# Performance work log

Hardware: AMD Instinct MI355X
Metric: run time of the kernel (lower is better)

## Reference

```python
import jax, jax.numpy as jnp
import numpy as np

N_GRID, N_MESH, N_EDGE, H = 65536, 10242, 131072, 512

def _layernorm(x, g, b, eps=1e-5):
    m = jnp.mean(x, axis=-1, keepdims=True)
    v = jnp.var(x, axis=-1, keepdims=True)
    return (x - m) * jax.lax.rsqrt(v + eps) * g + b

def _mlp(x, W1, b1, W2, b2, g, b):
    # Linear -> SiLU -> Linear -> LayerNorm (GraphCast MeshGraphMLP)
    h = jax.nn.silu(x @ W1 + b1)
    return _layernorm(h @ W2 + b2, g, b)

def setup_inputs() -> dict:
    key = jax.random.key(0)
    ks = jax.random.split(key, 16)
    s = lambda fan_in: 1.0 / np.sqrt(fan_in)
    inp = {
        'grid_node_features': jax.random.normal(ks[0], (N_GRID, H), jnp.float32),
        'mesh_node_features': jax.random.normal(ks[1], (N_MESH, H), jnp.float32),
        'grid2mesh_edge_features': jax.random.normal(ks[2], (N_EDGE, H), jnp.float32),
        'src_indices': jax.random.randint(ks[3], (N_EDGE,), 0, N_GRID),
        'dst_indices': jax.random.randint(ks[4], (N_EDGE,), 0, N_MESH),
        # edge MLP: in = concat(edge, src, dst) = 3H
        'We1': jax.random.normal(ks[5], (3 * H, H), jnp.float32) * s(3 * H),
        'be1': jnp.zeros((H,), jnp.float32),
        'We2': jax.random.normal(ks[6], (H, H), jnp.float32) * s(H),
        'be2': jnp.zeros((H,), jnp.float32),
        'ge': jnp.ones((H,), jnp.float32), 'bbe': jnp.zeros((H,), jnp.float32),
        # node MLP: in = concat(node, agg) = 2H
        'Wn1': jax.random.normal(ks[7], (2 * H, H), jnp.float32) * s(2 * H),
        'bn1': jnp.zeros((H,), jnp.float32),
        'Wn2': jax.random.normal(ks[8], (H, H), jnp.float32) * s(H),
        'bn2': jnp.zeros((H,), jnp.float32),
        'gn': jnp.ones((H,), jnp.float32), 'bbn': jnp.zeros((H,), jnp.float32),
        # grid node MLP: H -> H
        'Wg1': jax.random.normal(ks[9], (H, H), jnp.float32) * s(H),
        'bg1': jnp.zeros((H,), jnp.float32),
        'Wg2': jax.random.normal(ks[10], (H, H), jnp.float32) * s(H),
        'bg2': jnp.zeros((H,), jnp.float32),
        'gg': jnp.ones((H,), jnp.float32), 'bbg': jnp.zeros((H,), jnp.float32),
    }
    return inp

def reference(grid_node_features, mesh_node_features, grid2mesh_edge_features,
              src_indices, dst_indices,
              We1, be1, We2, be2, ge, bbe,
              Wn1, bn1, Wn2, bn2, gn, bbn,
              Wg1, bg1, Wg2, bg2, gg, bbg):
    # --- MeshEdgeBlock: gather src/dst, concat, MLP, residual on edges ---
    cat_e = jnp.concatenate([grid2mesh_edge_features,
                             grid_node_features[src_indices],
                             mesh_node_features[dst_indices]], axis=-1)  # [E, 3H]
    e_feats = grid2mesh_edge_features + _mlp(cat_e, We1, be1, We2, be2, ge, bbe)
    # --- MeshNodeBlock: scatter-sum edges to mesh nodes, concat, MLP ---
    agg = jax.ops.segment_sum(e_feats, dst_indices, num_segments=N_MESH)  # [M, H]
    cat_n = jnp.concatenate([mesh_node_features, agg], axis=-1)  # [M, 2H]
    n_feats = _mlp(cat_n, Wn1, bn1, Wn2, bn2, gn, bbn)
    mesh_out = mesh_node_features + n_feats
    # --- grid node MLP + residual ---
    grid_out = grid_node_features + _mlp(grid_node_features, Wg1, bg1, Wg2, bg2, gg, bbg)
    return (grid_out, mesh_out)
```

## Files before the change

kernel.cpp:

```cpp
#include <hip/hip_runtime.h>
#include <stdint.h>

typedef unsigned short u16;
typedef unsigned int   u32;
typedef unsigned char  u8;

using bf16x8 = __attribute__((ext_vector_type(8))) short;
using f32x4  = __attribute__((ext_vector_type(4))) float;

#define DEVF static __device__ __forceinline__

DEVF u16 f2bf(float f){
  u32 u = __builtin_bit_cast(u32, f);
  u32 r = u + 0x7FFFu + ((u >> 16) & 1u);
  return (u16)(r >> 16);
}
DEVF float bf2f(u16 h){
  u32 u = ((u32)h) << 16;
  return __builtin_bit_cast(float, u);
}

DEVF void gload_lds16(const u16* g, u16* s){
  __builtin_amdgcn_global_load_lds(
      (const __attribute__((address_space(1))) u32*)g,
      (__attribute__((address_space(3))) u32*)(u32)(uintptr_t)s,
      16, 0, 0);
}


__global__ __launch_bounds__(256) void k_f32_to_bf16(const float* __restrict__ in,
                                                     u16* __restrict__ out, long n){
  long i = (long)blockIdx.x * blockDim.x + threadIdx.x;
  long stride = (long)gridDim.x * blockDim.x;
  for (long j = i * 8; j < n; j += stride * 8){
    float4 a = *(const float4*)(in + j);
    float4 b = *(const float4*)(in + j + 4);
    bf16x8 v;
    v[0]=(short)f2bf(a.x); v[1]=(short)f2bf(a.y); v[2]=(short)f2bf(a.z); v[3]=(short)f2bf(a.w);
    v[4]=(short)f2bf(b.x); v[5]=(short)f2bf(b.y); v[6]=(short)f2bf(b.z); v[7]=(short)f2bf(b.w);
    *(bf16x8*)(out + j) = v;
  }
}

__global__ __launch_bounds__(256)
void k_conv_perm(const float* __restrict__ in, const int* __restrict__ pos,
                 u16* __restrict__ out, int E){
  int e = blockIdx.x * 4 + (threadIdx.x >> 6);
  int l = threadIdx.x & 63;
  if (e >= E) return;
  const float* r = in + (size_t)e * 512 + l * 8;
  float4 a = *(const float4*)r, b = *(const float4*)(r + 4);
  bf16x8 v;
  v[0]=(short)f2bf(a.x); v[1]=(short)f2bf(a.y); v[2]=(short)f2bf(a.z); v[3]=(short)f2bf(a.w);
  v[4]=(short)f2bf(b.x); v[5]=(short)f2bf(b.y); v[6]=(short)f2bf(b.z); v[7]=(short)f2bf(b.w);
  *(bf16x8*)(out + (size_t)pos[e] * 512 + l * 8) = v;
}

__global__ __launch_bounds__(256) void k_zero_i32(int* __restrict__ p, int n){
  int i = blockIdx.x * 256 + threadIdx.x;
  if (i < n) p[i] = 0;
}

__global__ __launch_bounds__(256) void k_transpose_w_off(const float* __restrict__ W,
                                                         u16* __restrict__ Wt,
                                                         int K, int N, int k0){
  int idx = blockIdx.x * 256 + threadIdx.x;
  if (idx < K * N){
    int k = idx / N, n = idx - k * N;
    Wt[(size_t)n * K + k] = f2bf(W[(size_t)(k + k0) * N + n]);
  }
}


__global__ __launch_bounds__(256)
void k_hist(const int* __restrict__ key, int* __restrict__ cnt, int E){
  int e = blockIdx.x * 256 + threadIdx.x;
  if (e < E) atomicAdd(&cnt[key[e]], 1);
}

__global__ __launch_bounds__(1024)
void k_scan(const int* __restrict__ cnt, int* __restrict__ offs, int n){
  __shared__ int part[1024];
  int t = threadIdx.x;
  const int PER = (n + 1023) / 1024;
  int base = t * PER;
  int s = 0;
  for (int i = 0; i < PER; ++i){ int idx = base + i; if (idx < n) s += cnt[idx]; }
  part[t] = s;
  __syncthreads();
  for (int o = 1; o < 1024; o <<= 1){
    int v = (t >= o) ? part[t - o] : 0;
    __syncthreads();
    part[t] += v;
    __syncthreads();
  }
  int run = (t == 0) ? 0 : part[t - 1];
  for (int i = 0; i < PER; ++i){
    int idx = base + i;
    if (idx < n){ offs[idx] = run; run += cnt[idx]; }
  }
  if (t == 1023) offs[n] = part[1023];
}

__global__ __launch_bounds__(256)
void k_scatter(const int* __restrict__ key, const int* __restrict__ offs,
               int* __restrict__ cur, int* __restrict__ eid, int E){
  int e = blockIdx.x * 256 + threadIdx.x;
  if (e < E){
    int d = key[e];
    int p = offs[d] + atomicAdd(&cur[d], 1);
    eid[p] = e;
  }
}

__global__ __launch_bounds__(256)
void k_scatter_pos(const int* __restrict__ key, const int* __restrict__ offs,
                   int* __restrict__ cur, int* __restrict__ eid,
                   int* __restrict__ pos, int E){
  int e = blockIdx.x * 256 + threadIdx.x;
  if (e < E){
    int d = key[e];
    int p = offs[d] + atomicAdd(&cur[d], 1);
    eid[p] = e;
    pos[e] = p;
  }
}

__global__ __launch_bounds__(256)
void k_make_idx(const int* __restrict__ eid_src, const int* __restrict__ src,
                const int* __restrict__ dst, int* __restrict__ srcS,
                int* __restrict__ dstS, int E){
  int r = blockIdx.x * 256 + threadIdx.x;
  if (r < E){ int e = eid_src[r]; srcS[r] = src[e]; dstS[r] = dst[e]; }
}

__global__ __launch_bounds__(256)
void k_compose(const int* __restrict__ eid_dst, const int* __restrict__ pos_src,
               int* __restrict__ eid_agg, int E){
  int p = blockIdx.x * 256 + threadIdx.x;
  if (p < E) eid_agg[p] = pos_src[eid_dst[p]];
}


#define LDA4(BUF, MH, KK, AF) \
  _Pragma("unroll") for (int m_ = 0; m_ < 4; ++m_) \
    AF[m_] = *(const bf16x8*)&lA[BUF][(wm * 128 + (MH) * 64 + m_ * 16 + lane16) * 64 + \
                                      ((((KK) << 2) | kl) ^ (lane16 & 7)) * 8];

#define LDB4(BUF, KK, BFR) \
  _Pragma("unroll") for (int n_ = 0; n_ < 4; ++n_) \
    BFR[n_] = *(const bf16x8*)&lB[BUF][(wn * 64 + n_ * 16 + lane16) * 64 + \
                                       ((((KK) << 2) | kl) ^ (lane16 & 7)) * 8];

#define PHASE_MFMA(MH, AF, BFR) \
  __builtin_amdgcn_s_setprio(1); \
  _Pragma("unroll") for (int m_ = 0; m_ < 4; ++m_) \
    _Pragma("unroll") for (int n_ = 0; n_ < 4; ++n_) \
      acc[(MH) * 4 + m_][n_] = __builtin_amdgcn_mfma_f32_16x16x32_bf16( \
          AF[m_], BFR[n_], acc[(MH) * 4 + m_][n_], 0, 0, 0); \
  __builtin_amdgcn_s_setprio(0);

#define STAGE_A(BUF, KT_, RND) do{ \
    const int k0_ = (KT_) * 64; \
    const u16* ga_; \
    if (MODE == 0){ ga_ = A + (size_t)srows[RND] * K + k0_ + kchunk; } \
    else { \
      int seg_ = k0_ >> 9, klo_ = k0_ & 511; \
      const u16* b_ = (seg_ == 0) ? A  + (size_t)srows[RND] * 512 \
                                  : G1 + (size_t)sidx1[RND] * 512; \
      ga_ = b_ + klo_ + kchunk; \
    } \
    gload_lds16(ga_, &lA[BUF][((RND) * 64 + w * 8) * 64]); \
  }while(0)

#define STAGE_B(BUF, KT_, RND) \
  gload_lds16(bptr[RND] + (KT_) * 64 + kchunk, &lB[BUF][((RND) * 64 + w * 8) * 64])

#define STAGE8(BUF, KT_) do{ \
    STAGE_A(BUF, KT_, 0); STAGE_A(BUF, KT_, 1); STAGE_A(BUF, KT_, 2); STAGE_A(BUF, KT_, 3); \
    STAGE_B(BUF, KT_, 0); STAGE_B(BUF, KT_, 1); STAGE_B(BUF, KT_, 2); STAGE_B(BUF, KT_, 3); \
  }while(0)

#define WAITBAR(N) do{ \
    asm volatile("s_waitcnt vmcnt(" #N ")" ::: "memory"); \
    __builtin_amdgcn_s_barrier(); \
    __builtin_amdgcn_sched_barrier(0); \
  }while(0)

template<int MODE, int EPI>
__global__ __launch_bounds__(512)
void k_gemm256(const u16* __restrict__ A, const u16* __restrict__ G1, const u16* __restrict__ G2,
               const int* __restrict__ srcI, const int* __restrict__ dstI,
               const u16* __restrict__ Bt, const float* __restrict__ bias,
               void* __restrict__ out, int M, int K)
{
  __shared__ __align__(16) u16 lA[2][256 * 64];
  __shared__ __align__(16) u16 lB[2][256 * 64];

  const int tid = threadIdx.x;
  const int w = tid >> 6, l = tid & 63;

  const int wgf = blockIdx.y * gridDim.x + blockIdx.x;
  const int pr = wgf >> 1, c = wgf & 1;
  const int npair = (gridDim.x * gridDim.y) >> 1;
  const int prs = (pr & 7) * (npair >> 3) + (pr >> 3);
  const int row0 = prs * 256;
  const int col0 = c * 256;

  int srows[4], sidx1[4];
  const u16* bptr[4];
  #pragma unroll
  for (int it = 0; it < 4; ++it){
    int r = row0 + it * 64 + w * 8 + (l >> 3);
    if (r >= M) r = M - 1;
    srows[it] = r;
    if (MODE == 1){ sidx1[it] = srcI[r]; }
    int n = col0 + it * 64 + w * 8 + (l >> 3);
    bptr[it] = Bt + (size_t)n * K;
  }
  const int kchunk = ((l & 7) ^ (l >> 3)) * 8;

  f32x4 acc[8][4];
  #pragma unroll
  for (int m = 0; m < 8; ++m)
    #pragma unroll
    for (int n = 0; n < 4; ++n)
      acc[m][n] = (f32x4){0.f, 0.f, 0.f, 0.f};

  const int wm = w >> 2, wn = w & 3;
  const int lane16 = l & 15, kl = l >> 4;

  const int KT = K >> 6;

  STAGE8(0, 0);

  for (int kt = 0; kt < KT; ++kt){
    const int buf = kt & 1;

    WAITBAR(0);

    if (kt + 1 < KT){ STAGE8(buf ^ 1, kt + 1); }
    __builtin_amdgcn_sched_barrier(0);

    bf16x8 af[4], bfr[4];
    LDB4(buf, 0, bfr);
    LDA4(buf, 0, 0, af);
    PHASE_MFMA(0, af, bfr);

    LDA4(buf, 1, 0, af);
    PHASE_MFMA(1, af, bfr);

    LDB4(buf, 1, bfr);
    LDA4(buf, 0, 1, af);
    PHASE_MFMA(0, af, bfr);

    LDA4(buf, 1, 1, af);
    PHASE_MFMA(1, af, bfr);
  }

  #pragma unroll
  for (int m = 0; m < 8; ++m){
    int rbase = row0 + wm * 128 + m * 16 + kl * 4;
    #pragma unroll
    for (int j = 0; j < 4; ++j){
      int rg = rbase + j;
      if (rg < M){
        int dd = 0;
        if (EPI == 3) dd = dstI[rg];
        #pragma unroll
        for (int n = 0; n < 4; ++n){
          int cg = col0 + wn * 64 + n * 16 + lane16;
          float v = acc[m][n][j];
          if (EPI == 0){
            v += bias[cg];
            v = v / (1.f + __expf(-v));
            ((u16*)out)[(size_t)rg * 512 + cg] = f2bf(v);
          } else if (EPI == 3){
            v += bias[cg] + bf2f(G2[(size_t)dd * 512 + cg]);
            v = v / (1.f + __expf(-v));
            ((u16*)out)[(size_t)rg * 512 + cg] = f2bf(v);
          } else if (EPI == 1){
            ((u16*)out)[(size_t)rg * 512 + cg] = f2bf(v);
          } else {
            ((float*)out)[(size_t)rg * 512 + cg] = v;
          }
        }
      }
    }
  }
}


template<int MODE, int EPI>
__global__ __launch_bounds__(256)
void k_gemm(const u16* __restrict__ A, const u16* __restrict__ G1, const u16* __restrict__ G2,
            const int* __restrict__ src, const int* __restrict__ dst,
            const u16* __restrict__ Bt, const float* __restrict__ bias,
            void* __restrict__ out, int M, int K)
{
  __shared__ __align__(16) u16 lA[128 * 64];
  __shared__ __align__(16) u16 lB[128 * 64];

  const int tid = threadIdx.x;
  const int w = tid >> 6, l = tid & 63;
  const int row0 = blockIdx.x * 128;
  const int col0 = blockIdx.y * 128;

  int srows[4];
  const u16* bptr[4];
  #pragma unroll
  for (int it = 0; it < 4; ++it){
    int r = row0 + it * 32 + w * 8 + (l >> 3);
    if (r >= M) r = M - 1;
    srows[it] = r;
    int n = col0 + it * 32 + w * 8 + (l >> 3);
    bptr[it] = Bt + (size_t)n * K;
  }
  const int kchunk = (l & 7) * 8;

  f32x4 acc[4][4];
  #pragma unroll
  for (int m = 0; m < 4; ++m)
    #pragma unroll
    for (int n = 0; n < 4; ++n)
      acc[m][n] = (f32x4){0.f, 0.f, 0.f, 0.f};

  const int wm = w >> 1, wn = w & 1;
  const int lane16 = l & 15, kl = l >> 4;

  const int KT = K >> 6;
  for (int kt = 0; kt < KT; ++kt){
    const int k0 = kt * 64;
    __syncthreads();
    #pragma unroll
    for (int it = 0; it < 4; ++it){
      const u16* ga;
      if (MODE == 0){
        ga = A + (size_t)srows[it] * K + k0 + kchunk;
      } else {
        int seg = k0 >> 9, klocal = k0 & 511;
        const u16* base = (seg == 0) ? A  + (size_t)srows[it] * 512
                                     : G1 + (size_t)srows[it] * 512;
        ga = base + klocal + kchunk;
      }
      gload_lds16(ga, &lA[(it * 32 + w * 8) * 64]);
      gload_lds16(bptr[it] + k0 + kchunk, &lB[(it * 32 + w * 8) * 64]);
    }
    __syncthreads();

    #pragma unroll
    for (int kk = 0; kk < 2; ++kk){
      bf16x8 af[4], bfr[4];
      #pragma unroll
      for (int m = 0; m < 4; ++m)
        af[m] = *(const bf16x8*)&lA[(wm * 64 + m * 16 + lane16) * 64 + kk * 32 + kl * 8];
      #pragma unroll
      for (int n = 0; n < 4; ++n)
        bfr[n] = *(const bf16x8*)&lB[(wn * 64 + n * 16 + lane16) * 64 + kk * 32 + kl * 8];
      #pragma unroll
      for (int m = 0; m < 4; ++m)
        #pragma unroll
        for (int n = 0; n < 4; ++n)
          acc[m][n] = __builtin_amdgcn_mfma_f32_16x16x32_bf16(af[m], bfr[n], acc[m][n], 0, 0, 0);
    }
  }

  #pragma unroll
  for (int m = 0; m < 4; ++m){
    int rbase = row0 + wm * 64 + m * 16 + kl * 4;
    #pragma unroll
    for (int n = 0; n < 4; ++n){
      int cg = col0 + wn * 64 + n * 16 + lane16;
      #pragma unroll
      for (int j = 0; j < 4; ++j){
        int rg = rbase + j;
        if (rg < M){
          float v = acc[m][n][j];
          if (EPI == 0){
            v += bias[cg];
            v = v / (1.f + __expf(-v));
            ((u16*)out)[(size_t)rg * 512 + cg] = f2bf(v);
          } else if (EPI == 1){
            ((u16*)out)[(size_t)rg * 512 + cg] = f2bf(v);
          } else {
            ((float*)out)[(size_t)rg * 512 + cg] = v;
          }
        }
      }
    }
  }
}


__global__ __launch_bounds__(256)
void k_agg(const u16* __restrict__ e2, const float* __restrict__ be2,
           const float* __restrict__ ge, const float* __restrict__ bbe,
           const float* __restrict__ edge_f, const int* __restrict__ offs,
           const int* __restrict__ eid_d, const int* __restrict__ eid_a,
           u16* __restrict__ aggbf, int Mn)
{
  int node = blockIdx.x * 4 + (threadIdx.x >> 6);
  int l = threadIdx.x & 63;
  if (node >= Mn) return;
  int p0 = offs[node], p1 = offs[node + 1];

  float b2c[8], gc[8], bbc[8];
  #pragma unroll
  for (int j = 0; j < 8; ++j){
    int c = l * 8 + j;
    b2c[j] = be2[c]; gc[j] = ge[c]; bbc[j] = bbe[c];
  }

  float acc[8] = {0.f,0.f,0.f,0.f,0.f,0.f,0.f,0.f};
  for (int p = p0; p < p1; ++p){
    int e = eid_d[p];
    int q = eid_a[p];
    bf16x8 v = *(const bf16x8*)(e2 + (size_t)q * 512 + l * 8);
    const float* ei = edge_f + (size_t)e * 512 + l * 8;
    float4 a = *(const float4*)ei, b4 = *(const float4*)(ei + 4);
    float eiv[8] = {a.x, a.y, a.z, a.w, b4.x, b4.y, b4.z, b4.w};
    float x[8], s = 0.f, sq = 0.f;
    #pragma unroll
    for (int j = 0; j < 8; ++j){
      x[j] = bf2f((u16)v[j]) + b2c[j];
      s += x[j]; sq += x[j] * x[j];
    }
    #pragma unroll
    for (int o = 32; o; o >>= 1){ s += __shfl_xor(s, o); sq += __shfl_xor(sq, o); }
    float mean = s * (1.f / 512.f);
    float var = sq * (1.f / 512.f) - mean * mean;
    float rs = rsqrtf(var + 1e-5f);
    #pragma unroll
    for (int j = 0; j < 8; ++j)
      acc[j] += (x[j] - mean) * rs * gc[j] + bbc[j] + eiv[j];
  }

  bf16x8 o8;
  #pragma unroll
  for (int j = 0; j < 8; ++j) o8[j] = (short)f2bf(acc[j]);
  *(bf16x8*)(aggbf + (size_t)node * 512 + l * 8) = o8;
}


__global__ __launch_bounds__(256)
void k_ln_out(const float* __restrict__ x2, const float* __restrict__ b2,
              const float* __restrict__ g, const float* __restrict__ bb,
              const float* __restrict__ resid, float* __restrict__ out, int R)
{
  int row = blockIdx.x * 4 + (threadIdx.x >> 6);
  int l = threadIdx.x & 63;
  if (row >= R) return;
  const float* xr = x2 + (size_t)row * 512 + l * 8;
  float4 a = *(const float4*)xr, b4 = *(const float4*)(xr + 4);
  float x[8] = {a.x, a.y, a.z, a.w, b4.x, b4.y, b4.z, b4.w};
  float s = 0.f, sq = 0.f;
  #pragma unroll
  for (int j = 0; j < 8; ++j){
    x[j] += b2[l * 8 + j];
    s += x[j]; sq += x[j] * x[j];
  }
  #pragma unroll
  for (int o = 32; o; o >>= 1){ s += __shfl_xor(s, o); sq += __shfl_xor(sq, o); }
  float mean = s * (1.f / 512.f);
  float var = sq * (1.f / 512.f) - mean * mean;
  float rs = rsqrtf(var + 1e-5f);
  const float* rr = resid + (size_t)row * 512 + l * 8;
  float* po = out + (size_t)row * 512 + l * 8;
  #pragma unroll
  for (int j = 0; j < 8; ++j){
    int c = l * 8 + j;
    po[j] = (x[j] - mean) * rs * g[c] + bb[c] + rr[j];
  }
}

__global__ __launch_bounds__(256)
void k_ln_out_bb(const u16* __restrict__ x2, const float* __restrict__ b2,
                 const float* __restrict__ g, const float* __restrict__ bb,
                 const u16* __restrict__ resid, float* __restrict__ out, int R)
{
  int row = blockIdx.x * 4 + (threadIdx.x >> 6);
  int l = threadIdx.x & 63;
  if (row >= R) return;
  bf16x8 xv = *(const bf16x8*)(x2 + (size_t)row * 512 + l * 8);
  float x[8], s = 0.f, sq = 0.f;
  #pragma unroll
  for (int j = 0; j < 8; ++j){
    x[j] = bf2f((u16)xv[j]) + b2[l * 8 + j];
    s += x[j]; sq += x[j] * x[j];
  }
  #pragma unroll
  for (int o = 32; o; o >>= 1){ s += __shfl_xor(s, o); sq += __shfl_xor(sq, o); }
  float mean = s * (1.f / 512.f);
  float var = sq * (1.f / 512.f) - mean * mean;
  float rs = rsqrtf(var + 1e-5f);
  bf16x8 rv = *(const bf16x8*)(resid + (size_t)row * 512 + l * 8);
  float* po = out + (size_t)row * 512 + l * 8;
  #pragma unroll
  for (int j = 0; j < 8; ++j){
    int c = l * 8 + j;
    po[j] = (x[j] - mean) * rs * g[c] + bb[c] + bf2f((u16)rv[j]);
  }
}


extern "C" void kernel_launch(void* const* d_in, const int* in_sizes, int n_in,
                              void* d_out, int out_size, void* d_ws, size_t ws_size,
                              hipStream_t stream)
{
  const int N_GRID = 65536, N_MESH = 10242, N_EDGE = 131072, H = 512;

  const float* grid_f = (const float*)d_in[0];
  const float* mesh_f = (const float*)d_in[1];
  const float* edge_f = (const float*)d_in[2];
  const int*   src    = (const int*)d_in[3];
  const int*   dst    = (const int*)d_in[4];
  const float* We1 = (const float*)d_in[5];  const float* be1 = (const float*)d_in[6];
  const float* We2 = (const float*)d_in[7];  const float* be2 = (const float*)d_in[8];
  const float* ge  = (const float*)d_in[9];  const float* bbe = (const float*)d_in[10];
  const float* Wn1 = (const float*)d_in[11]; const float* bn1 = (const float*)d_in[12];
  const float* Wn2 = (const float*)d_in[13]; const float* bn2 = (const float*)d_in[14];
  const float* gn  = (const float*)d_in[15]; const float* bbn = (const float*)d_in[16];
  const float* Wg1 = (const float*)d_in[17]; const float* bg1 = (const float*)d_in[18];
  const float* Wg2 = (const float*)d_in[19]; const float* bg2 = (const float*)d_in[20];
  const float* gg  = (const float*)d_in[21]; const float* bbg = (const float*)d_in[22];

  u8* ws = (u8*)d_ws;
  const size_t MiB = 1u << 20;
  u16*  Gbf   = (u16*)(ws + 0);
  u16*  Mbf   = (u16*)(ws + 64  * MiB);
  u16*  AggBf = (u16*)(ws + 75  * MiB);
  u16*  We1t  = (u16*)(ws + 86  * MiB);
  u16*  Wpm   = (u16*)(ws + 86  * MiB + 1048576);
  u16*  We2t  = (u16*)(ws + 86  * MiB + 1572864);
  u16*  Wn1t  = (u16*)(ws + 86  * MiB + 2097152);
  u16*  Wn2t  = (u16*)(ws + 86  * MiB + 3145728);
  u16*  Wg1t  = (u16*)(ws + 86  * MiB + 3670016);
  u16*  Wg2t  = (u16*)(ws + 86  * MiB + 4194304);
  int*  offs_d = (int*)(ws + 91 * MiB);
  int*  cnt_d  = (int*)(ws + 91 * MiB) + 10496;
  int*  cur_d  = (int*)(ws + 91 * MiB) + 20992;
  int*  eid_d  = (int*)(ws + 91 * MiB) + 31488;
  int*  offs_s = (int*)(ws + 92 * MiB);
  int*  cnt_s  = (int*)(ws + 92 * MiB) + 65792;
  int*  cur_s  = (int*)(ws + 92 * MiB) + 131328;
  int*  eid_s  = (int*)(ws + 92 * MiB) + 196864;
  int*  pos_s  = (int*)(ws + 92 * MiB) + 327936;
  int*  srcS   = (int*)(ws + 92 * MiB) + 459008;
  int*  dstS   = (int*)(ws + 92 * MiB) + 590080;
  int*  eid_a  = (int*)(ws + 92 * MiB) + 721152;
  u16*  Pm    = (u16*)(ws + 96 * MiB);
  u16*  He    = (u16*)(ws + 112 * MiB);
  u8*   Big   =  ws + 240 * MiB;
  u16*  Ebf   = (u16*)Big;
  u16*  E2    = (u16*)Big;
  float* N2   = (float*)Big;
  u16*  G2    = (u16*)Big;

  float* grid_out = (float*)d_out;
  float* mesh_out = (float*)d_out + (size_t)N_GRID * H;

  k_zero_i32<<<(20992 + 255) / 256, 256, 0, stream>>>(cnt_d, 20992);
  k_zero_i32<<<(131072 + 255) / 256, 256, 0, stream>>>(cnt_s, 131072);
  k_hist<<<N_EDGE / 256, 256, 0, stream>>>(dst, cnt_d, N_EDGE);
  k_hist<<<N_EDGE / 256, 256, 0, stream>>>(src, cnt_s, N_EDGE);
  k_scan<<<1, 1024, 0, stream>>>(cnt_d, offs_d, N_MESH);
  k_scan<<<1, 1024, 0, stream>>>(cnt_s, offs_s, N_GRID);
  k_scatter<<<N_EDGE / 256, 256, 0, stream>>>(dst, offs_d, cur_d, eid_d, N_EDGE);
  k_scatter_pos<<<N_EDGE / 256, 256, 0, stream>>>(src, offs_s, cur_s, eid_s, pos_s, N_EDGE);
  k_make_idx<<<N_EDGE / 256, 256, 0, stream>>>(eid_s, src, dst, srcS, dstS, N_EDGE);
  k_compose<<<N_EDGE / 256, 256, 0, stream>>>(eid_d, pos_s, eid_a, N_EDGE);

  k_f32_to_bf16<<<2048, 256, 0, stream>>>(grid_f, Gbf, (long)N_GRID * H);
  k_f32_to_bf16<<<1024, 256, 0, stream>>>(mesh_f, Mbf, (long)N_MESH * H);
  k_conv_perm<<<N_EDGE / 4, 256, 0, stream>>>(edge_f, pos_s, Ebf, N_EDGE);
  k_transpose_w_off<<<(1024 * 512 + 255) / 256, 256, 0, stream>>>(We1, We1t, 1024, 512, 0);
  k_transpose_w_off<<<(512  * 512 + 255) / 256, 256, 0, stream>>>(We1, Wpm, 512, 512, 1024);
  k_transpose_w_off<<<(512  * 512 + 255) / 256, 256, 0, stream>>>(We2, We2t, 512, 512, 0);
  k_transpose_w_off<<<(1024 * 512 + 255) / 256, 256, 0, stream>>>(Wn1, Wn1t, 1024, 512, 0);
  k_transpose_w_off<<<(512  * 512 + 255) / 256, 256, 0, stream>>>(Wn2, Wn2t, 512, 512, 0);
  k_transpose_w_off<<<(512  * 512 + 255) / 256, 256, 0, stream>>>(Wg1, Wg1t, 512, 512, 0);
  k_transpose_w_off<<<(512  * 512 + 255) / 256, 256, 0, stream>>>(Wg2, Wg2t, 512, 512, 0);

  dim3 gpm((N_MESH + 127) / 128, 4);
  k_gemm<0, 1><<<gpm, 256, 0, stream>>>(Mbf, nullptr, nullptr, nullptr, nullptr, Wpm, nullptr, Pm, N_MESH, 512);

  dim3 ge1(2, N_EDGE / 256);
  k_gemm256<1, 3><<<ge1, 512, 0, stream>>>(Ebf, Gbf, Pm, srcS, dstS, We1t, be1, He, N_EDGE, 1024);
  k_gemm256<0, 1><<<ge1, 512, 0, stream>>>(He, nullptr, nullptr, nullptr, nullptr, We2t, nullptr, E2, N_EDGE, 512);
  k_agg<<<(N_MESH + 3) / 4, 256, 0, stream>>>(E2, be2, ge, bbe, edge_f, offs_d, eid_d, eid_a, AggBf, N_MESH);

  dim3 gn1((N_MESH + 127) / 128, 4);
  k_gemm<1, 0><<<gn1, 256, 0, stream>>>(Mbf, AggBf, nullptr, nullptr, nullptr, Wn1t, bn1, He, N_MESH, 1024);
  k_gemm<0, 2><<<gn1, 256, 0, stream>>>(He, nullptr, nullptr, nullptr, nullptr, Wn2t, nullptr, N2, N_MESH, 512);
  k_ln_out<<<(N_MESH + 3) / 4, 256, 0, stream>>>(N2, bn2, gn, bbn, mesh_f, mesh_out, N_MESH);

  dim3 gg1(2, N_GRID / 256);
  k_gemm256<0, 0><<<gg1, 512, 0, stream>>>(Gbf, nullptr, nullptr, nullptr, nullptr, Wg1t, bg1, He, N_GRID, 512);
  k_gemm256<0, 1><<<gg1, 512, 0, stream>>>(He, nullptr, nullptr, nullptr, nullptr, Wg2t, nullptr, G2, N_GRID, 512);
  k_ln_out_bb<<<N_GRID / 4, 256, 0, stream>>>(G2, bg2, gg, bbg, Gbf, grid_out, N_GRID);
}
```

Before: 1.089 ms.

## Sort edges by destination only and change GEMM workgroup swizzle

Edges are now ordered by destination mesh node instead of by source grid node. This removes the second histogram, scan and scatter passes and the composed index, and lets the aggregation read edge-MLP outputs contiguously. The source-node gather in the first edge GEMM becomes random rather than sorted, so grid-feature reads lose locality. The gemm256 workgroup-to-tile mapping is also changed to a generic XCD-interleaved swizzle over both grid dimensions.

```diff
diff --git a/kernel.cpp b/kernel.cpp
--- a/kernel.cpp
+++ b/kernel.cpp
@@ -103,17 +103,6 @@
 }
 
 __global__ __launch_bounds__(256)
-void k_scatter(const int* __restrict__ key, const int* __restrict__ offs,
-               int* __restrict__ cur, int* __restrict__ eid, int E){
-  int e = blockIdx.x * 256 + threadIdx.x;
-  if (e < E){
-    int d = key[e];
-    int p = offs[d] + atomicAdd(&cur[d], 1);
-    eid[p] = e;
-  }
-}
-
-__global__ __launch_bounds__(256)
 void k_scatter_pos(const int* __restrict__ key, const int* __restrict__ offs,
                    int* __restrict__ cur, int* __restrict__ eid,
                    int* __restrict__ pos, int E){
@@ -127,18 +116,11 @@
 }
 
 __global__ __launch_bounds__(256)
-void k_make_idx(const int* __restrict__ eid_src, const int* __restrict__ src,
-                const int* __restrict__ dst, int* __restrict__ srcS,
-                int* __restrict__ dstS, int E){
+void k_make_idx(const int* __restrict__ eid_d, const int* __restrict__ src,
+                const int* __restrict__ dst, int* __restrict__ srcD,
+                int* __restrict__ dstD, int E){
   int r = blockIdx.x * 256 + threadIdx.x;
-  if (r < E){ int e = eid_src[r]; srcS[r] = src[e]; dstS[r] = dst[e]; }
-}
-
-__global__ __launch_bounds__(256)
-void k_compose(const int* __restrict__ eid_dst, const int* __restrict__ pos_src,
-               int* __restrict__ eid_agg, int E){
-  int p = blockIdx.x * 256 + threadIdx.x;
-  if (p < E) eid_agg[p] = pos_src[eid_dst[p]];
+  if (r < E){ int e = eid_d[r]; srcD[r] = src[e]; dstD[r] = dst[e]; }
 }
 
 
@@ -200,12 +182,11 @@
   const int tid = threadIdx.x;
   const int w = tid >> 6, l = tid & 63;
 
+  const int nwg = gridDim.x * gridDim.y;
   const int wgf = blockIdx.y * gridDim.x + blockIdx.x;
-  const int pr = wgf >> 1, c = wgf & 1;
-  const int npair = (gridDim.x * gridDim.y) >> 1;
-  const int prs = (pr & 7) * (npair >> 3) + (pr >> 3);
-  const int row0 = prs * 256;
-  const int col0 = c * 256;
+  const int lg  = (wgf & 7) * (nwg >> 3) + (wgf >> 3);
+  const int col0 = (lg % gridDim.x) * 256;
+  const int row0 = (lg / gridDim.x) * 256;
 
   int srows[4], sidx1[4];
   const u16* bptr[4];
@@ -396,8 +377,7 @@
 void k_agg(const u16* __restrict__ e2, const float* __restrict__ be2,
            const float* __restrict__ ge, const float* __restrict__ bbe,
            const float* __restrict__ edge_f, const int* __restrict__ offs,
-           const int* __restrict__ eid_d, const int* __restrict__ eid_a,
-           u16* __restrict__ aggbf, int Mn)
+           const int* __restrict__ eid_d, u16* __restrict__ aggbf, int Mn)
 {
   int node = blockIdx.x * 4 + (threadIdx.x >> 6);
   int l = threadIdx.x & 63;
@@ -413,10 +393,8 @@
 
   float acc[8] = {0.f,0.f,0.f,0.f,0.f,0.f,0.f,0.f};
   for (int p = p0; p < p1; ++p){
-    int e = eid_d[p];
-    int q = eid_a[p];
-    bf16x8 v = *(const bf16x8*)(e2 + (size_t)q * 512 + l * 8);
-    const float* ei = edge_f + (size_t)e * 512 + l * 8;
+    bf16x8 v = *(const bf16x8*)(e2 + (size_t)p * 512 + l * 8);
+    const float* ei = edge_f + (size_t)eid_d[p] * 512 + l * 8;
     float4 a = *(const float4*)ei, b4 = *(const float4*)(ei + 4);
     float eiv[8] = {a.x, a.y, a.z, a.w, b4.x, b4.y, b4.z, b4.w};
     float x[8], s = 0.f, sq = 0.f;
@@ -540,14 +518,9 @@
   int*  cnt_d  = (int*)(ws + 91 * MiB) + 10496;
   int*  cur_d  = (int*)(ws + 91 * MiB) + 20992;
   int*  eid_d  = (int*)(ws + 91 * MiB) + 31488;
-  int*  offs_s = (int*)(ws + 92 * MiB);
-  int*  cnt_s  = (int*)(ws + 92 * MiB) + 65792;
-  int*  cur_s  = (int*)(ws + 92 * MiB) + 131328;
-  int*  eid_s  = (int*)(ws + 92 * MiB) + 196864;
-  int*  pos_s  = (int*)(ws + 92 * MiB) + 327936;
-  int*  srcS   = (int*)(ws + 92 * MiB) + 459008;
-  int*  dstS   = (int*)(ws + 92 * MiB) + 590080;
-  int*  eid_a  = (int*)(ws + 92 * MiB) + 721152;
+  int*  pos_d  = (int*)(ws + 92 * MiB);
+  int*  srcD   = (int*)(ws + 92 * MiB) + 131072;
+  int*  dstD   = (int*)(ws + 92 * MiB) + 262144;
   u16*  Pm    = (u16*)(ws + 96 * MiB);
   u16*  He    = (u16*)(ws + 112 * MiB);
   u8*   Big   =  ws + 240 * MiB;
@@ -560,19 +533,14 @@
   float* mesh_out = (float*)d_out + (size_t)N_GRID * H;
 
   k_zero_i32<<<(20992 + 255) / 256, 256, 0, stream>>>(cnt_d, 20992);
-  k_zero_i32<<<(131072 + 255) / 256, 256, 0, stream>>>(cnt_s, 131072);
   k_hist<<<N_EDGE / 256, 256, 0, stream>>>(dst, cnt_d, N_EDGE);
-  k_hist<<<N_EDGE / 256, 256, 0, stream>>>(src, cnt_s, N_EDGE);
   k_scan<<<1, 1024, 0, stream>>>(cnt_d, offs_d, N_MESH);
-  k_scan<<<1, 1024, 0, stream>>>(cnt_s, offs_s, N_GRID);
-  k_scatter<<<N_EDGE / 256, 256, 0, stream>>>(dst, offs_d, cur_d, eid_d, N_EDGE);
-  k_scatter_pos<<<N_EDGE / 256, 256, 0, stream>>>(src, offs_s, cur_s, eid_s, pos_s, N_EDGE);
-  k_make_idx<<<N_EDGE / 256, 256, 0, stream>>>(eid_s, src, dst, srcS, dstS, N_EDGE);
-  k_compose<<<N_EDGE / 256, 256, 0, stream>>>(eid_d, pos_s, eid_a, N_EDGE);
+  k_scatter_pos<<<N_EDGE / 256, 256, 0, stream>>>(dst, offs_d, cur_d, eid_d, pos_d, N_EDGE);
+  k_make_idx<<<N_EDGE / 256, 256, 0, stream>>>(eid_d, src, dst, srcD, dstD, N_EDGE);
 
   k_f32_to_bf16<<<2048, 256, 0, stream>>>(grid_f, Gbf, (long)N_GRID * H);
   k_f32_to_bf16<<<1024, 256, 0, stream>>>(mesh_f, Mbf, (long)N_MESH * H);
-  k_conv_perm<<<N_EDGE / 4, 256, 0, stream>>>(edge_f, pos_s, Ebf, N_EDGE);
+  k_conv_perm<<<N_EDGE / 4, 256, 0, stream>>>(edge_f, pos_d, Ebf, N_EDGE);
   k_transpose_w_off<<<(1024 * 512 + 255) / 256, 256, 0, stream>>>(We1, We1t, 1024, 512, 0);
   k_transpose_w_off<<<(512  * 512 + 255) / 256, 256, 0, stream>>>(We1, Wpm, 512, 512, 1024);
   k_transpose_w_off<<<(512  * 512 + 255) / 256, 256, 0, stream>>>(We2, We2t, 512, 512, 0);
@@ -585,9 +553,9 @@
   k_gemm<0, 1><<<gpm, 256, 0, stream>>>(Mbf, nullptr, nullptr, nullptr, nullptr, Wpm, nullptr, Pm, N_MESH, 512);
 
   dim3 ge1(2, N_EDGE / 256);
-  k_gemm256<1, 3><<<ge1, 512, 0, stream>>>(Ebf, Gbf, Pm, srcS, dstS, We1t, be1, He, N_EDGE, 1024);
+  k_gemm256<1, 3><<<ge1, 512, 0, stream>>>(Ebf, Gbf, Pm, srcD, dstD, We1t, be1, He, N_EDGE, 1024);
   k_gemm256<0, 1><<<ge1, 512, 0, stream>>>(He, nullptr, nullptr, nullptr, nullptr, We2t, nullptr, E2, N_EDGE, 512);
-  k_agg<<<(N_MESH + 3) / 4, 256, 0, stream>>>(E2, be2, ge, bbe, edge_f, offs_d, eid_d, eid_a, AggBf, N_MESH);
+  k_agg<<<(N_MESH + 3) / 4, 256, 0, stream>>>(E2, be2, ge, bbe, edge_f, offs_d, eid_d, AggBf, N_MESH);
 
   dim3 gn1((N_MESH + 127) / 128, 4);
   k_gemm<1, 0><<<gn1, 256, 0, stream>>>(Mbf, AggBf, nullptr, nullptr, nullptr, Wn1t, bn1, He, N_MESH, 1024);
```

New measurement: 939.2 us. 13.7% less time.
